# Optimization experiments

Measured on AMD Instinct MI355X. Metric: run time of the kernel, lower is better.

The kernel has to match this reference:

```python
import jax, jax.numpy as jnp
import numpy as np

B = 256
M = (32, 32, 32)          # size_in modes
N = (32, 32, 32)          # size_out modes
R = (1, 16, 16, 1)        # TT ranks
CORE_SCALE = 0.05


def setup_inputs() -> dict:
    key = jax.random.key(0)
    kx, k0, k1, k2, kb = jax.random.split(key, 5)
    x = jax.random.normal(kx, (B,) + M, dtype=jnp.float32)
    # TT cores: core_i has shape [r_i, n_i, m_i, r_{i+1}]
    core0 = jax.random.normal(k0, (R[0], N[0], M[0], R[1]), dtype=jnp.float32) * CORE_SCALE
    core1 = jax.random.normal(k1, (R[1], N[1], M[1], R[2]), dtype=jnp.float32) * CORE_SCALE
    core2 = jax.random.normal(k2, (R[2], N[2], M[2], R[3]), dtype=jnp.float32) * CORE_SCALE
    bias = jax.random.normal(kb, N, dtype=jnp.float32) * 0.01
    return {"x": x, "core0": core0, "core1": core1, "core2": core2, "bias": bias}


def _tt_matvec(x, cores):
    # y[..., n1..nd] = sum_{m1..md} prod_i core_i[r_i, n_i, m_i, r_{i+1}] * x[..., m1..md]
    d = len(cores)
    batch_shape = x.shape[:-d]
    # z: [B, r, P, m_i, m_{i+1}, ..., m_d]  (P = flattened already-produced n dims)
    z = x.reshape((-1, 1, 1) + x.shape[-d:])
    n_dims = []
    for core in cores:
        r, n, m, s = core.shape
        # contract current input mode m and left rank r; append output mode n
        z = jnp.einsum('rnms,brpm...->bspn...', core, z)
        n_dims.append(n)
        sh = z.shape
        z = z.reshape(sh[:2] + (sh[2] * sh[3],) + sh[4:])  # merge P and n
    return z.reshape(batch_shape + tuple(n_dims))


def reference(x, core0, core1, core2, bias):
    y = _tt_matvec(x, (core0, core1, core2))
    return y + bias
```

## Files before the change

### kernel.cpp

```cpp
#include <hip/hip_runtime.h>
#include <hip/hip_bf16.h>


typedef __attribute__((ext_vector_type(8)))  short bf16x8;
typedef __attribute__((ext_vector_type(4)))  float f32x4;
typedef __attribute__((ext_vector_type(16))) float f32x16;

#define WS_A1   0
#define WS_A0T  262144
#define WS_W2T  278528

__device__ __forceinline__ unsigned short f2bf(float f) {
    union { float f; unsigned int u; } v; v.f = f;
    unsigned int u = v.u;
    u += 0x7fffu + ((u >> 16) & 1u);
    return (unsigned short)(u >> 16);
}

__device__ __forceinline__ unsigned int cvt2(float a, float b) {
    union { __hip_bfloat162 h; unsigned int u; } v;
    v.h = __float22bfloat162_rn(float2{a, b});
    return v.u;
}

__global__ void tt_prep(const float* __restrict__ core0,
                        const float* __restrict__ core1,
                        const float* __restrict__ core2,
                        unsigned short* __restrict__ ws)
{
    const int u = blockIdx.x * 256 + threadIdx.x;
    unsigned short* A1  = ws + WS_A1;
    unsigned short* A0T = ws + WS_A0T;
    unsigned short* W2T = ws + WS_W2T;
    bf16x8 o;
    if (u < 32768) {
        int e = u * 8;
        int row = e >> 9, col0 = e & 511;
        int n2 = row >> 4, s = row & 15;
        int m2 = col0 >> 4, r0 = col0 & 15;
        const float* src = core1 + n2 * 512 + m2 * 16 + s;
        #pragma unroll
        for (int j = 0; j < 8; ++j) o[j] = (short)f2bf(src[(r0 + j) * 16384]);
        *(bf16x8*)(A1 + e) = o;
    } else if (u < 34816) {
        int e = (u - 32768) * 8;
        int row = e >> 5, m1b = e & 31;
        int n1 = row >> 4, s = row & 15;
        const float* src = core0 + n1 * 512 + m1b * 16 + s;
        #pragma unroll
        for (int j = 0; j < 8; ++j) o[j] = (short)f2bf(src[j * 16]);
        *(bf16x8*)(A0T + e) = o;
    } else if (u < 36864) {
        int e = (u - 34816) * 8;
        int n3 = e >> 9, k20 = e & 511;
        int m3 = k20 >> 4, s0 = k20 & 15;
        const float* src = core2 + n3 * 32 + m3;
        #pragma unroll
        for (int j = 0; j < 8; ++j) o[j] = (short)f2bf(src[(s0 + j) * 1024]);
        *(bf16x8*)(W2T + e) = o;
    }
}

__global__ __launch_bounds__(512, 2)
void tt_mfma(const float* __restrict__ x,
             const unsigned short* __restrict__ ws,
             const float* __restrict__ bias,
             float* __restrict__ out)
{
    extern __shared__ char smem[];

    const unsigned short* A1  = ws + WS_A1;
    const unsigned short* A0T = ws + WS_A0T;
    const unsigned short* W2T = ws + WS_W2T;

    const int t   = threadIdx.x;
    const int l   = t & 63;
    const int w   = t >> 6;
    const int l15 = l & 15;
    const int lg  = l >> 4;

    const int swzid = (blockIdx.x & 7) * 256 + (blockIdx.x >> 3);
    const int bq = swzid >> 5;
    const int n1 = swzid & 31;

    const int swz5 = ((l15 >> 1) & 1) << 5;

    {
        const int lb = w >> 1, ph = w & 1;
        const int b  = bq * 4 + lb;
        char* zb = smem + lb * 32768;
        bf16x8 afrag = *(const bf16x8*)(A0T + n1 * 512 + l15 * 32 + lg * 8);
        const float* xb = x + (size_t)b * 32768 + lg * 8192 + ph * 512 + l15;
        #pragma unroll 2
        for (int pti = 0; pti < 32; ++pti) {
            const float* xp = xb + pti * 16;
            float v0 = xp[0],    v1 = xp[1024], v2 = xp[2048], v3 = xp[3072];
            float v4 = xp[4096], v5 = xp[5120], v6 = xp[6144], v7 = xp[7168];
            uint4 hh;
            hh.x = cvt2(v0, v1); hh.y = cvt2(v2, v3);
            hh.z = cvt2(v4, v5); hh.w = cvt2(v6, v7);
            bf16x8 bfrag = *(bf16x8*)&hh;
            f32x4 c = __builtin_amdgcn_mfma_f32_16x16x32_bf16(
                afrag, bfrag, (f32x4){0.f, 0.f, 0.f, 0.f}, 0, 0, 0);
            int p = ph * 512 + pti * 16 + l15;
            int m2 = p >> 5, m3 = p & 31;
            uint2 h;
            h.x = cvt2(c[0], c[1]);
            h.y = cvt2(c[2], c[3]);
            int off = ((m2 >> 1) << 11) + (m3 << 6) +
                      ((((m2 & 1) << 5) + (lg << 3)) ^ (((m3 >> 1) & 1) << 5));
            *(uint2*)(zb + off) = h;
        }
    }
    __syncthreads();

    f32x16 acc[2][4];
    #pragma unroll
    for (int mt = 0; mt < 2; ++mt)
        #pragma unroll
        for (int nt = 0; nt < 4; ++nt)
            acc[mt][nt] = (f32x16){0.f,0.f,0.f,0.f,0.f,0.f,0.f,0.f,
                                   0.f,0.f,0.f,0.f,0.f,0.f,0.f,0.f};
    const int c31 = l & 31;
    const int hi  = l >> 5;
    {
        const unsigned short* a1p = A1 + (size_t)(w * 64 + c31) * 512 + hi * 8;
        const int zsw = ((c31 >> 1) & 1) << 5;
        const int zco = c31 << 6;
        #pragma unroll 4
        for (int step = 0; step < 32; ++step) {
            bf16x8 af0 = *(const bf16x8*)(a1p + step * 16);
            bf16x8 af1 = *(const bf16x8*)(a1p + 16384 + step * 16);
            int zoff = ((step >> 1) << 11) + zco +
                       ((((step & 1) << 5) + (hi << 4)) ^ zsw);
            bf16x8 b0 = *(const bf16x8*)(smem + zoff);
            bf16x8 b1 = *(const bf16x8*)(smem + 32768  + zoff);
            bf16x8 b2 = *(const bf16x8*)(smem + 65536  + zoff);
            bf16x8 b3 = *(const bf16x8*)(smem + 98304  + zoff);
            acc[0][0] = __builtin_amdgcn_mfma_f32_32x32x16_bf16(af0, b0, acc[0][0], 0, 0, 0);
            acc[0][1] = __builtin_amdgcn_mfma_f32_32x32x16_bf16(af0, b1, acc[0][1], 0, 0, 0);
            acc[0][2] = __builtin_amdgcn_mfma_f32_32x32x16_bf16(af0, b2, acc[0][2], 0, 0, 0);
            acc[0][3] = __builtin_amdgcn_mfma_f32_32x32x16_bf16(af0, b3, acc[0][3], 0, 0, 0);
            acc[1][0] = __builtin_amdgcn_mfma_f32_32x32x16_bf16(af1, b0, acc[1][0], 0, 0, 0);
            acc[1][1] = __builtin_amdgcn_mfma_f32_32x32x16_bf16(af1, b1, acc[1][1], 0, 0, 0);
            acc[1][2] = __builtin_amdgcn_mfma_f32_32x32x16_bf16(af1, b2, acc[1][2], 0, 0, 0);
            acc[1][3] = __builtin_amdgcn_mfma_f32_32x32x16_bf16(af1, b3, acc[1][3], 0, 0, 0);
        }
    }
    __syncthreads();

    {
        #pragma unroll
        for (int mt = 0; mt < 2; ++mt) {
            #pragma unroll
            for (int nt = 0; nt < 4; ++nt) {
                char* zb = smem + nt * 32768;
                #pragma unroll
                for (int g = 0; g < 4; ++g) {
                    int n2 = w * 4 + mt * 2 + (g >> 1);
                    uint2 h;
                    h.x = cvt2(acc[mt][nt][4 * g],     acc[mt][nt][4 * g + 1]);
                    h.y = cvt2(acc[mt][nt][4 * g + 2], acc[mt][nt][4 * g + 3]);
                    int inoff = (((c31 & 1) << 5) + (hi << 3) + ((g & 1) << 4)) ^
                                (((n2 >> 1) & 1) << 5);
                    int off = ((c31 >> 1) << 11) + (n2 << 6) + inoff;
                    *(uint2*)(zb + off) = h;
                }
            }
        }
    }
    __syncthreads();

    {
        const int lb = w >> 1, n3h = w & 1;
        const int b  = bq * 4 + lb;
        char* zb = smem + lb * 32768;
        f32x4 c[2];
        c[0] = (f32x4){0.f, 0.f, 0.f, 0.f};
        c[1] = (f32x4){0.f, 0.f, 0.f, 0.f};
        const unsigned short* w2p = W2T + (n3h * 16 + l15) * 512 + lg * 8;
        const int kofs = (lg << 4) ^ swz5;
        #pragma unroll 4
        for (int ks = 0; ks < 16; ++ks) {
            bf16x8 bfg = *(const bf16x8*)(w2p + ks * 32);
            #pragma unroll
            for (int mt = 0; mt < 2; ++mt) {
                int n2 = mt * 16 + l15;
                bf16x8 af = *(const bf16x8*)(zb + ks * 2048 + (n2 << 6) + kofs);
                c[mt] = __builtin_amdgcn_mfma_f32_16x16x32_bf16(af, bfg, c[mt], 0, 0, 0);
            }
        }
        int n3 = n3h * 16 + l15;
        size_t ob = (size_t)b * 32768 + (size_t)n1 * 1024;
        const float* bp2 = bias + n1 * 1024;
        #pragma unroll
        for (int mt = 0; mt < 2; ++mt)
            #pragma unroll
            for (int i = 0; i < 4; ++i) {
                int n2 = mt * 16 + lg * 4 + i;
                out[ob + n2 * 32 + n3] = c[mt][i] + bp2[n2 * 32 + n3];
            }
    }
}

extern "C" void kernel_launch(void* const* d_in, const int* in_sizes, int n_in,
                              void* d_out, int out_size, void* d_ws, size_t ws_size,
                              hipStream_t stream) {
    (void)in_sizes; (void)n_in; (void)out_size; (void)ws_size;
    const float* x     = (const float*)d_in[0];
    const float* core0 = (const float*)d_in[1];
    const float* core1 = (const float*)d_in[2];
    const float* core2 = (const float*)d_in[3];
    const float* bias  = (const float*)d_in[4];
    float* out = (float*)d_out;
    unsigned short* ws = (unsigned short*)d_ws;

    const int lds_bytes = 4 * 32768;
    hipFuncSetAttribute((const void*)tt_mfma,
                        hipFuncAttributeMaxDynamicSharedMemorySize, lds_bytes);
    tt_prep<<<144, 256, 0, stream>>>(core0, core1, core2, ws);
    tt_mfma<<<2048, 512, lds_bytes, stream>>>(x, ws, bias, out);
}
```

Baseline: 256.1 us.

## Pre-transpose x to bf16 in workspace and software-pipeline fragment loads

Adds a prep pass that converts x to bf16 and transposes it so the m1 mode is innermost. This lets the first-stage MFMA load each B fragment as one contiguous 16-byte read instead of eight strided fp32 loads, and the next fragment is prefetched through double buffering. It also double-buffers the W2T fragment loads in the last stage. The cost is an extra pass over x (read fp32, write bf16) and a dependency on workspace size, with a fallback path kept when the workspace is too small.

```diff
diff --git a/kernel.cpp b/kernel.cpp
--- a/kernel.cpp
+++ b/kernel.cpp
@@ -9,6 +9,9 @@
 #define WS_A1   0
 #define WS_A0T  262144
 #define WS_W2T  278528
+#define WS_XT   294912
+#define WS_XT_ELEMS 8388608
+#define WS_NEED_BYTES ((size_t)(WS_XT + WS_XT_ELEMS) * 2)
 
 __device__ __forceinline__ unsigned short f2bf(float f) {
     union { float f; unsigned int u; } v; v.f = f;
@@ -23,12 +26,36 @@
     return v.u;
 }
 
-__global__ void tt_prep(const float* __restrict__ core0,
+template<bool XT>
+__global__ void tt_prep(const float* __restrict__ x,
+                        const float* __restrict__ core0,
                         const float* __restrict__ core1,
                         const float* __restrict__ core2,
                         unsigned short* __restrict__ ws)
 {
-    const int u = blockIdx.x * 256 + threadIdx.x;
+    const int t = threadIdx.x;
+    if (XT && blockIdx.x < 8192) {
+        __shared__ float tile[32 * 36];
+        const int b  = blockIdx.x >> 5;
+        const int m2 = blockIdx.x & 31;
+        {
+            const int m1 = t >> 3, c4 = (t & 7) * 4;
+            float4 v = *(const float4*)(x + (size_t)b * 32768 + m1 * 1024 + m2 * 32 + c4);
+            *(float4*)&tile[m1 * 36 + c4] = v;
+        }
+        __syncthreads();
+        {
+            const int m3 = t >> 3, g = t & 7;
+            unsigned short o[4];
+            #pragma unroll
+            for (int j = 0; j < 4; ++j)
+                o[j] = f2bf(tile[(g * 4 + j) * 36 + m3]);
+            unsigned short* dst = ws + WS_XT + (size_t)b * 32768 + (m2 * 32 + m3) * 32 + g * 4;
+            *(uint2*)dst = *(uint2*)o;
+        }
+        return;
+    }
+    const int u = (blockIdx.x - (XT ? 8192 : 0)) * 256 + t;
     unsigned short* A1  = ws + WS_A1;
     unsigned short* A0T = ws + WS_A0T;
     unsigned short* W2T = ws + WS_W2T;
@@ -61,6 +88,7 @@
     }
 }
 
+template<bool XT>
 __global__ __launch_bounds__(512, 2)
 void tt_mfma(const float* __restrict__ x,
              const unsigned short* __restrict__ ws,
@@ -72,6 +100,7 @@
     const unsigned short* A1  = ws + WS_A1;
     const unsigned short* A0T = ws + WS_A0T;
     const unsigned short* W2T = ws + WS_W2T;
+    const unsigned short* xT  = ws + WS_XT;
 
     const int t   = threadIdx.x;
     const int l   = t & 63;
@@ -90,26 +119,44 @@
         const int b  = bq * 4 + lb;
         char* zb = smem + lb * 32768;
         bf16x8 afrag = *(const bf16x8*)(A0T + n1 * 512 + l15 * 32 + lg * 8);
-        const float* xb = x + (size_t)b * 32768 + lg * 8192 + ph * 512 + l15;
-        #pragma unroll 2
-        for (int pti = 0; pti < 32; ++pti) {
-            const float* xp = xb + pti * 16;
-            float v0 = xp[0],    v1 = xp[1024], v2 = xp[2048], v3 = xp[3072];
-            float v4 = xp[4096], v5 = xp[5120], v6 = xp[6144], v7 = xp[7168];
-            uint4 hh;
-            hh.x = cvt2(v0, v1); hh.y = cvt2(v2, v3);
-            hh.z = cvt2(v4, v5); hh.w = cvt2(v6, v7);
-            bf16x8 bfrag = *(bf16x8*)&hh;
-            f32x4 c = __builtin_amdgcn_mfma_f32_16x16x32_bf16(
-                afrag, bfrag, (f32x4){0.f, 0.f, 0.f, 0.f}, 0, 0, 0);
-            int p = ph * 512 + pti * 16 + l15;
-            int m2 = p >> 5, m3 = p & 31;
-            uint2 h;
-            h.x = cvt2(c[0], c[1]);
-            h.y = cvt2(c[2], c[3]);
-            int off = ((m2 >> 1) << 11) + (m3 << 6) +
-                      ((((m2 & 1) << 5) + (lg << 3)) ^ (((m3 >> 1) & 1) << 5));
-            *(uint2*)(zb + off) = h;
+        if (XT) {
+            const unsigned short* xb = xT + (size_t)b * 32768 + lg * 8;
+            bf16x8 bfrag[2];
+            bfrag[0] = *(const bf16x8*)(xb + (ph * 512 + l15) * 32);
+            #pragma unroll
+            for (int pti = 0; pti < 32; ++pti) {
+                if (pti < 31) {
+                    int pn = ph * 512 + (pti + 1) * 16 + l15;
+                    bfrag[(pti + 1) & 1] = *(const bf16x8*)(xb + pn * 32);
+                }
+                int p = ph * 512 + pti * 16 + l15;
+                f32x4 c = __builtin_amdgcn_mfma_f32_16x16x32_bf16(
+                    afrag, bfrag[pti & 1], (f32x4){0.f, 0.f, 0.f, 0.f}, 0, 0, 0);
+                int m2 = p >> 5, m3 = p & 31;
+                uint2 h;
+                h.x = cvt2(c[0], c[1]);
+                h.y = cvt2(c[2], c[3]);
+                int off = ((m2 >> 1) << 11) + (m3 << 6) +
+                          ((((m2 & 1) << 5) + (lg << 3)) ^ (((m3 >> 1) & 1) << 5));
+                *(uint2*)(zb + off) = h;
+            }
+        } else {
+            const float* xb = x + (size_t)b * 32768 + (lg * 8) * 1024;
+            for (int pti = 0; pti < 32; ++pti) {
+                int p = ph * 512 + pti * 16 + l15;
+                bf16x8 bfrag;
+                #pragma unroll
+                for (int j = 0; j < 8; ++j) bfrag[j] = (short)f2bf(xb[j * 1024 + p]);
+                f32x4 c = __builtin_amdgcn_mfma_f32_16x16x32_bf16(
+                    afrag, bfrag, (f32x4){0.f, 0.f, 0.f, 0.f}, 0, 0, 0);
+                int m2 = p >> 5, m3 = p & 31;
+                uint2 h;
+                h.x = cvt2(c[0], c[1]);
+                h.y = cvt2(c[2], c[3]);
+                int off = ((m2 >> 1) << 11) + (m3 << 6) +
+                          ((((m2 & 1) << 5) + (lg << 3)) ^ (((m3 >> 1) & 1) << 5));
+                *(uint2*)(zb + off) = h;
+            }
         }
     }
     __syncthreads();
@@ -180,14 +227,16 @@
         c[1] = (f32x4){0.f, 0.f, 0.f, 0.f};
         const unsigned short* w2p = W2T + (n3h * 16 + l15) * 512 + lg * 8;
         const int kofs = (lg << 4) ^ swz5;
-        #pragma unroll 4
+        bf16x8 bfg[2];
+        bfg[0] = *(const bf16x8*)(w2p);
+        #pragma unroll
         for (int ks = 0; ks < 16; ++ks) {
-            bf16x8 bfg = *(const bf16x8*)(w2p + ks * 32);
+            if (ks < 15) bfg[(ks + 1) & 1] = *(const bf16x8*)(w2p + (ks + 1) * 32);
             #pragma unroll
             for (int mt = 0; mt < 2; ++mt) {
                 int n2 = mt * 16 + l15;
                 bf16x8 af = *(const bf16x8*)(zb + ks * 2048 + (n2 << 6) + kofs);
-                c[mt] = __builtin_amdgcn_mfma_f32_16x16x32_bf16(af, bfg, c[mt], 0, 0, 0);
+                c[mt] = __builtin_amdgcn_mfma_f32_16x16x32_bf16(af, bfg[ks & 1], c[mt], 0, 0, 0);
             }
         }
         int n3 = n3h * 16 + l15;
@@ -206,7 +255,7 @@
 extern "C" void kernel_launch(void* const* d_in, const int* in_sizes, int n_in,
                               void* d_out, int out_size, void* d_ws, size_t ws_size,
                               hipStream_t stream) {
-    (void)in_sizes; (void)n_in; (void)out_size; (void)ws_size;
+    (void)in_sizes; (void)n_in; (void)out_size;
     const float* x     = (const float*)d_in[0];
     const float* core0 = (const float*)d_in[1];
     const float* core1 = (const float*)d_in[2];
@@ -216,8 +265,15 @@
     unsigned short* ws = (unsigned short*)d_ws;
 
     const int lds_bytes = 4 * 32768;
-    hipFuncSetAttribute((const void*)tt_mfma,
-                        hipFuncAttributeMaxDynamicSharedMemorySize, lds_bytes);
-    tt_prep<<<144, 256, 0, stream>>>(core0, core1, core2, ws);
-    tt_mfma<<<2048, 512, lds_bytes, stream>>>(x, ws, bias, out);
-}
+    if (ws_size >= WS_NEED_BYTES) {
+        hipFuncSetAttribute((const void*)tt_mfma<true>,
+                            hipFuncAttributeMaxDynamicSharedMemorySize, lds_bytes);
+        tt_prep<true><<<8336, 256, 0, stream>>>(x, core0, core1, core2, ws);
+        tt_mfma<true><<<2048, 512, lds_bytes, stream>>>(x, ws, bias, out);
+    } else {
+        hipFuncSetAttribute((const void*)tt_mfma<false>,
+                            hipFuncAttributeMaxDynamicSharedMemorySize, lds_bytes);
+        tt_prep<false><<<144, 256, 0, stream>>>(x, core0, core1, core2, ws);
+        tt_mfma<false><<<2048, 512, lds_bytes, stream>>>(x, ws, bias, out);
+    }
+}
```

Result: faster. 229.2 us (-10.5%).
